# Kernel tuning notes

Measured on AMD Instinct MI355X. Metric: run time of the kernel, lower is better.

The kernel has to match this reference:

```python
import jax, jax.numpy as jnp
import numpy as np

N = 10000   # nodes
E = 320000  # edges
G = 64      # graphs in batch
D = 256     # gnn embedding dim
A = 118     # atomic_num_dim
OUT = 100   # spectrum dim
NUM_GINE = 2


def setup_inputs() -> dict:
    key = jax.random.key(0)
    ks = jax.random.split(key, 16)
    inp = {
        'atomic_num': jax.random.normal(ks[0], (N, A), dtype=jnp.float32),
        'length': jax.random.uniform(ks[1], (E,), dtype=jnp.float32),
        'src': jax.random.randint(ks[2], (E,), 0, N, dtype=jnp.int32),
        'dst': jax.random.randint(ks[3], (E,), 0, N, dtype=jnp.int32),
        'graph_ids': jnp.sort(jax.random.randint(ks[4], (N,), 0, G, dtype=jnp.int32)),
        # parameters
        'W_node': jax.random.normal(ks[5], (A, D), dtype=jnp.float32) / np.sqrt(A),
        'b_node': jnp.zeros((D,), dtype=jnp.float32),
        'W_edge': jax.random.normal(ks[6], (1, D), dtype=jnp.float32),
        'b_edge': jnp.zeros((D,), dtype=jnp.float32),
        'gine_eps': jnp.zeros((NUM_GINE,), dtype=jnp.float32),  # learnable eps per GINEConv
        'W_gnn': jax.random.normal(ks[7], (NUM_GINE, D, D), dtype=jnp.float32) / np.sqrt(D),
        'b_gnn': jnp.zeros((NUM_GINE, D), dtype=jnp.float32),
        'eps_param': jnp.array([1e-3], dtype=jnp.float32),  # unify_vector eps
        'W_mlp': jax.random.normal(ks[8], (D, OUT), dtype=jnp.float32) / np.sqrt(D),
        'b_mlp': jnp.zeros((OUT,), dtype=jnp.float32),
    }
    return inp


def reference(atomic_num, length, src, dst, graph_ids,
              W_node, b_node, W_edge, b_edge,
              gine_eps, W_gnn, b_gnn, eps_param, W_mlp, b_mlp):
    # node / edge embeddings
    h = atomic_num @ W_node + b_node            # [N, D]
    e = length[:, None] @ W_edge + b_edge       # [E, D]
    # GINEConv layers: m_ij = relu(h_src + e_ij); h_i' = W((1+eps)h_i + sum_j m_ij) + b
    for i in range(NUM_GINE):
        m = jax.nn.relu(h[src] + e)             # [E, D] gather + elementwise
        agg = jax.ops.segment_sum(m, dst, num_segments=N)  # scatter-sum to dst nodes
        h = ((1.0 + gine_eps[i]) * h + agg) @ W_gnn[i] + b_gnn[i]
    # sum_nodes pooling per graph
    feat = jax.ops.segment_sum(h, graph_ids, num_segments=G)  # [G, D]
    # unify_vector: global min/max normalization
    mn = jnp.min(feat)
    mx = jnp.max(feat)
    feat = (feat - mn) / (eps_param[0] + mx - mn)
    # MLP head (no hidden layers): Linear(D, 100)
    return feat @ W_mlp + b_mlp                 # [G, 100]
```

## Files before the change

kernel.cpp:

```cpp
#include <hip/hip_runtime.h>
#include <hip/hip_bf16.h>

#define N_NODES 10000
#define N_EDGES 320000
#define N_GRAPHS 64
#define DIM 256
#define HALF_D 128
#define ADIM 118
#define OUTD 100
#define CAP 192

typedef short bf8_t __attribute__((ext_vector_type(8)));
typedef float f4_t  __attribute__((ext_vector_type(4)));

__device__ __forceinline__ unsigned short f2bf(float f) {
    unsigned u = __float_as_uint(f);
    u += 0x7FFFu + ((u >> 16) & 1u);
    return (unsigned short)(u >> 16);
}
__device__ __forceinline__ float bf2f(unsigned short s) {
    return __uint_as_float(((unsigned)s) << 16);
}

__global__ __launch_bounds__(256) void convW_k(
    const float* __restrict__ Wn, const float* __restrict__ Wg,
    unsigned short* __restrict__ WnT, unsigned short* __restrict__ WgT,
    int* __restrict__ cursor, float* __restrict__ feat) {
    int i = blockIdx.x * 256 + threadIdx.x;
    if (i < 32768) {
        int c = i >> 7, k = i & 127;
        WnT[i] = (k < ADIM) ? f2bf(Wn[k * DIM + c]) : (unsigned short)0;
    } else {
        int j = i - 32768;
        int l = j >> 16, rem = j & 65535;
        int c = rem >> 8, k = rem & 255;
        WgT[j] = f2bf(Wg[l * 65536 + k * DIM + c]);
    }
    if (i < N_NODES) cursor[i] = i * CAP;
    if (i < N_GRAPHS * DIM) feat[i] = 0.f;
}

__global__ __launch_bounds__(256) void fill_k(
    const int* __restrict__ src, const int* __restrict__ dst,
    const float* __restrict__ len, int* __restrict__ cursor,
    int2* __restrict__ epack) {
    int j = blockIdx.x * 256 + threadIdx.x;
    if (j >= N_EDGES) return;
    int d = dst[j];
    int pos = atomicAdd(&cursor[d], 1);
    if (pos < d * CAP + CAP)
        epack[pos] = make_int2(src[j], __float_as_int(len[j]));
}

#define AST 136
__global__ __launch_bounds__(256) void node_embed_k(
    const float* __restrict__ an, const unsigned short* __restrict__ WnT,
    const float* __restrict__ bn, unsigned short* __restrict__ hbf) {
    __shared__ unsigned short xs[16 * AST];
    const int base = blockIdx.x * 16;
    const int tid = threadIdx.x;
    for (int i = tid; i < 16 * (AST - ADIM); i += 256) {
        int r = i / (AST - ADIM);
        int c = i - r * (AST - ADIM);
        xs[r * AST + ADIM + c] = 0;
    }
    for (int i = tid; i < 16 * ADIM; i += 256) {
        int r = i / ADIM;
        int c = i - r * ADIM;
        xs[r * AST + c] = f2bf(an[(size_t)(base + r) * ADIM + c]);
    }
    __syncthreads();
    const int wave = tid >> 6, lane = tid & 63;
    const int m = lane & 15, quad = lane >> 4;
    bf8_t afrag[4];
    #pragma unroll
    for (int s = 0; s < 4; ++s)
        afrag[s] = *(const bf8_t*)&xs[m * AST + s * 32 + quad * 8];
    const int colbase = wave * 64;
    f4_t acc[4];
    #pragma unroll
    for (int ct = 0; ct < 4; ++ct) acc[ct] = (f4_t){0.f, 0.f, 0.f, 0.f};
    #pragma unroll
    for (int ct = 0; ct < 4; ++ct) {
        const unsigned short* wp = WnT + (size_t)(colbase + ct * 16 + m) * 128 + quad * 8;
        #pragma unroll
        for (int s = 0; s < 4; ++s) {
            bf8_t bfrag = *(const bf8_t*)(wp + s * 32);
            acc[ct] = __builtin_amdgcn_mfma_f32_16x16x32_bf16(afrag[s], bfrag, acc[ct], 0, 0, 0);
        }
    }
    #pragma unroll
    for (int ct = 0; ct < 4; ++ct) {
        int col = colbase + ct * 16 + m;
        float bb = bn[col];
        unsigned short* hp = hbf + (size_t)(col >> 7) * N_NODES * HALF_D + (col & 127);
        #pragma unroll
        for (int r = 0; r < 4; ++r)
            hp[(size_t)(base + quad * 4 + r) * HALF_D] = f2bf(acc[ct][r] + bb);
    }
}

__global__ __launch_bounds__(256) void gather_k(
    const unsigned short* __restrict__ hbf, const int* __restrict__ cursor,
    const int2* __restrict__ epack, const float* __restrict__ We,
    const float* __restrict__ be, const float* __restrict__ epsp, int layer,
    unsigned short* __restrict__ xbf) {
    const int wave = threadIdx.x >> 6, lane = threadIdx.x & 63;
    const int q = blockIdx.x >> 3, r = blockIdx.x & 7;
    const int half = r >> 2;
    const int node = __builtin_amdgcn_readfirstlane((q * 4 + (r & 3)) * 4 + wave);
    const int d = half * HALF_D + lane * 2;
    const unsigned short* hb = hbf + (size_t)half * N_NODES * HALF_D + lane * 2;
    const float2 w  = *(const float2*)(We + d);
    const float2 bb = *(const float2*)(be + d);
    float2 acc = {0.f, 0.f};
    const int lo = node * CAP;
    const int cnt = min(__builtin_amdgcn_readfirstlane(cursor[node]) - lo, CAP);
    const int2* ep = epack + lo;
    int t = 0;
    for (; t + 7 < cnt; t += 8) {
        int2 p0 = ep[t + 0], p1 = ep[t + 1], p2 = ep[t + 2], p3 = ep[t + 3];
        int2 p4 = ep[t + 4], p5 = ep[t + 5], p6 = ep[t + 6], p7 = ep[t + 7];
        ushort2 a0 = *(const ushort2*)(hb + (size_t)p0.x * HALF_D);
        ushort2 a1 = *(const ushort2*)(hb + (size_t)p1.x * HALF_D);
        ushort2 a2 = *(const ushort2*)(hb + (size_t)p2.x * HALF_D);
        ushort2 a3 = *(const ushort2*)(hb + (size_t)p3.x * HALF_D);
        ushort2 a4 = *(const ushort2*)(hb + (size_t)p4.x * HALF_D);
        ushort2 a5 = *(const ushort2*)(hb + (size_t)p5.x * HALF_D);
        ushort2 a6 = *(const ushort2*)(hb + (size_t)p6.x * HALF_D);
        ushort2 a7 = *(const ushort2*)(hb + (size_t)p7.x * HALF_D);
        float l0 = __int_as_float(p0.y), l1 = __int_as_float(p1.y);
        float l2 = __int_as_float(p2.y), l3 = __int_as_float(p3.y);
        float l4 = __int_as_float(p4.y), l5 = __int_as_float(p5.y);
        float l6 = __int_as_float(p6.y), l7 = __int_as_float(p7.y);
        acc.x += fmaxf(bf2f(a0.x) + fmaf(l0, w.x, bb.x), 0.f);
        acc.y += fmaxf(bf2f(a0.y) + fmaf(l0, w.y, bb.y), 0.f);
        acc.x += fmaxf(bf2f(a1.x) + fmaf(l1, w.x, bb.x), 0.f);
        acc.y += fmaxf(bf2f(a1.y) + fmaf(l1, w.y, bb.y), 0.f);
        acc.x += fmaxf(bf2f(a2.x) + fmaf(l2, w.x, bb.x), 0.f);
        acc.y += fmaxf(bf2f(a2.y) + fmaf(l2, w.y, bb.y), 0.f);
        acc.x += fmaxf(bf2f(a3.x) + fmaf(l3, w.x, bb.x), 0.f);
        acc.y += fmaxf(bf2f(a3.y) + fmaf(l3, w.y, bb.y), 0.f);
        acc.x += fmaxf(bf2f(a4.x) + fmaf(l4, w.x, bb.x), 0.f);
        acc.y += fmaxf(bf2f(a4.y) + fmaf(l4, w.y, bb.y), 0.f);
        acc.x += fmaxf(bf2f(a5.x) + fmaf(l5, w.x, bb.x), 0.f);
        acc.y += fmaxf(bf2f(a5.y) + fmaf(l5, w.y, bb.y), 0.f);
        acc.x += fmaxf(bf2f(a6.x) + fmaf(l6, w.x, bb.x), 0.f);
        acc.y += fmaxf(bf2f(a6.y) + fmaf(l6, w.y, bb.y), 0.f);
        acc.x += fmaxf(bf2f(a7.x) + fmaf(l7, w.x, bb.x), 0.f);
        acc.y += fmaxf(bf2f(a7.y) + fmaf(l7, w.y, bb.y), 0.f);
    }
    for (; t < cnt; ++t) {
        int2 p0 = ep[t];
        ushort2 a0 = *(const ushort2*)(hb + (size_t)p0.x * HALF_D);
        float l0 = __int_as_float(p0.y);
        acc.x += fmaxf(bf2f(a0.x) + fmaf(l0, w.x, bb.x), 0.f);
        acc.y += fmaxf(bf2f(a0.y) + fmaf(l0, w.y, bb.y), 0.f);
    }
    const float eps1 = 1.f + epsp[layer];
    ushort2 hv = *(const ushort2*)(hb + (size_t)node * HALF_D);
    ushort2 o;
    o.x = f2bf(fmaf(eps1, bf2f(hv.x), acc.x));
    o.y = f2bf(fmaf(eps1, bf2f(hv.y), acc.y));
    *(ushort2*)(xbf + (size_t)half * N_NODES * HALF_D + (size_t)node * HALF_D + lane * 2) = o;
}

#define XST 264
__global__ __launch_bounds__(256) void update_k(
    const unsigned short* __restrict__ xbf,
    const unsigned short* __restrict__ WT, const float* __restrict__ b,
    unsigned short* __restrict__ hout,
    const int* __restrict__ gid, float* __restrict__ feat, int do_pool) {
    __shared__ unsigned short xs[16 * XST];
    __shared__ int gids[16];
    const int base = blockIdx.x * 16;
    const int tid = threadIdx.x;
    #pragma unroll
    for (int cch = tid; cch < 512; cch += 256) {
        int rr = cch >> 5, k0 = (cch & 31) * 8;
        const unsigned short* sp = xbf + (size_t)(k0 >> 7) * N_NODES * HALF_D
                                 + (size_t)(base + rr) * HALF_D + (k0 & 127);
        *(bf8_t*)&xs[rr * XST + k0] = *(const bf8_t*)sp;
    }
    if (do_pool && tid < 16) gids[tid] = gid[base + tid];
    __syncthreads();
    const int wave = tid >> 6, lane = tid & 63;
    const int m = lane & 15, quad = lane >> 4;
    bf8_t afrag[8];
    #pragma unroll
    for (int s = 0; s < 8; ++s)
        afrag[s] = *(const bf8_t*)&xs[m * XST + s * 32 + quad * 8];
    const int colbase = wave * 64;
    f4_t acc[4];
    #pragma unroll
    for (int ct = 0; ct < 4; ++ct) acc[ct] = (f4_t){0.f, 0.f, 0.f, 0.f};
    #pragma unroll
    for (int ct = 0; ct < 4; ++ct) {
        const unsigned short* wp = WT + (size_t)(colbase + ct * 16 + m) * DIM + quad * 8;
        #pragma unroll
        for (int s = 0; s < 8; ++s) {
            bf8_t bfrag = *(const bf8_t*)(wp + s * 32);
            acc[ct] = __builtin_amdgcn_mfma_f32_16x16x32_bf16(afrag[s], bfrag, acc[ct], 0, 0, 0);
        }
    }
    if (!do_pool) {
        #pragma unroll
        for (int ct = 0; ct < 4; ++ct) {
            int col = colbase + ct * 16 + m;
            float bb = b[col];
            unsigned short* hp = hout + (size_t)(col >> 7) * N_NODES * HALF_D + (col & 127);
            #pragma unroll
            for (int r = 0; r < 4; ++r)
                hp[(size_t)(base + quad * 4 + r) * HALF_D] = f2bf(acc[ct][r] + bb);
        }
    } else {
        #pragma unroll
        for (int ct = 0; ct < 4; ++ct) {
            int col = colbase + ct * 16 + m;
            float bb = b[col];
            float run = 0.f;
            int cur = gids[quad * 4];
            #pragma unroll
            for (int r = 0; r < 4; ++r) {
                int g = gids[quad * 4 + r];
                if (g != cur) {
                    atomicAdd(&feat[(size_t)cur * DIM + col], run);
                    run = 0.f;
                    cur = g;
                }
                run += acc[ct][r] + bb;
            }
            atomicAdd(&feat[(size_t)cur * DIM + col], run);
        }
    }
}

__global__ __launch_bounds__(256) void headmm_k(
    const float* __restrict__ feat, const float* __restrict__ Wm,
    const float* __restrict__ bm, const float* __restrict__ epsp,
    float* __restrict__ out) {
    __shared__ float frow[DIM];
    __shared__ float smn[4], smx[4], sMn, sMx;
    const int g = blockIdx.x;
    const int tid = threadIdx.x;
    float mn = 3.4e38f, mx = -3.4e38f;
    for (int i = tid; i < N_GRAPHS * DIM; i += 256) {
        float v = feat[i];
        mn = fminf(mn, v);
        mx = fmaxf(mx, v);
    }
    frow[tid] = feat[g * DIM + tid];
    #pragma unroll
    for (int off = 32; off > 0; off >>= 1) {
        mn = fminf(mn, __shfl_down(mn, off, 64));
        mx = fmaxf(mx, __shfl_down(mx, off, 64));
    }
    const int wave = tid >> 6, lane = tid & 63;
    if (lane == 0) { smn[wave] = mn; smx[wave] = mx; }
    __syncthreads();
    if (tid == 0) {
        sMn = fminf(fminf(smn[0], smn[1]), fminf(smn[2], smn[3]));
        sMx = fmaxf(fmaxf(smx[0], smx[1]), fmaxf(smx[2], smx[3]));
    }
    __syncthreads();
    if (tid < OUTD) {
        const float mnv = sMn;
        const float inv = 1.f / (epsp[0] + sMx - mnv);
        float acc = 0.f;
        for (int d = 0; d < DIM; ++d)
            acc += (frow[d] - mnv) * Wm[d * OUTD + tid];
        out[g * OUTD + tid] = acc * inv + bm[tid];
    }
}

extern "C" void kernel_launch(void* const* d_in, const int* in_sizes, int n_in,
                              void* d_out, int out_size, void* d_ws, size_t ws_size,
                              hipStream_t stream) {
    const float* atomic_num = (const float*)d_in[0];
    const float* length     = (const float*)d_in[1];
    const int*   src        = (const int*)d_in[2];
    const int*   dst        = (const int*)d_in[3];
    const int*   gid        = (const int*)d_in[4];
    const float* W_node     = (const float*)d_in[5];
    const float* b_node     = (const float*)d_in[6];
    const float* W_edge     = (const float*)d_in[7];
    const float* b_edge     = (const float*)d_in[8];
    const float* gine_eps   = (const float*)d_in[9];
    const float* W_gnn      = (const float*)d_in[10];
    const float* b_gnn      = (const float*)d_in[11];
    const float* eps_param  = (const float*)d_in[12];
    const float* W_mlp      = (const float*)d_in[13];
    const float* b_mlp      = (const float*)d_in[14];
    float* out = (float*)d_out;

    float* feat = (float*)d_ws;
    int* cursor = (int*)(feat + (size_t)N_GRAPHS * DIM);
    int2* epack = (int2*)(cursor + N_NODES + 4);
    unsigned short* hbf0 = (unsigned short*)(epack + (size_t)N_NODES * CAP);
    unsigned short* hbf1 = hbf0 + (size_t)N_NODES * DIM;
    unsigned short* xbf  = hbf1 + (size_t)N_NODES * DIM;
    unsigned short* WnT  = xbf + (size_t)N_NODES * DIM;
    unsigned short* WgT  = WnT + 256 * 128;

    convW_k<<<640, 256, 0, stream>>>(W_node, W_gnn, WnT, WgT, cursor, feat);
    fill_k<<<N_EDGES / 256, 256, 0, stream>>>(src, dst, length, cursor, epack);
    node_embed_k<<<N_NODES / 16, 256, 0, stream>>>(atomic_num, WnT, b_node, hbf0);

    gather_k<<<N_NODES / 2, 256, 0, stream>>>(
        hbf0, cursor, epack, W_edge, b_edge, gine_eps, 0, xbf);
    update_k<<<N_NODES / 16, 256, 0, stream>>>(
        xbf, WgT, b_gnn, hbf1, gid, feat, 0);
    gather_k<<<N_NODES / 2, 256, 0, stream>>>(
        hbf1, cursor, epack, W_edge, b_edge, gine_eps, 1, xbf);
    update_k<<<N_NODES / 16, 256, 0, stream>>>(
        xbf, WgT + 256 * 256, b_gnn + DIM, hbf0, gid, feat, 1);

    headmm_k<<<N_GRAPHS, 256, 0, stream>>>(feat, W_mlp, b_mlp, eps_param, out);
}
```

Measured before the change: 217.4 us.

## Switch node features to row-major layout and split edges across waves per node

Node feature buffers move from a split-half column layout to plain row-major [N, 256] bf16. The gather kernel now gives each node its own block: the four waves each take a quarter of the node's edges, each lane loads 4 contiguous bf16 values per edge, and the partial sums are reduced through shared memory. The update kernel splits each 16-row tile across two blocks, each computing 128 output columns, to raise parallelism. The aim is wider, full-row gathers and better load balance across waves, paid for with an extra shared-memory reduction, a barrier per node and twice as many gather blocks.

```diff
diff --git a/kernel.cpp b/kernel.cpp
--- a/kernel.cpp
+++ b/kernel.cpp
@@ -5,7 +5,6 @@
 #define N_EDGES 320000
 #define N_GRAPHS 64
 #define DIM 256
-#define HALF_D 128
 #define ADIM 118
 #define OUTD 100
 #define CAP 192
@@ -93,10 +92,9 @@
     for (int ct = 0; ct < 4; ++ct) {
         int col = colbase + ct * 16 + m;
         float bb = bn[col];
-        unsigned short* hp = hbf + (size_t)(col >> 7) * N_NODES * HALF_D + (col & 127);
         #pragma unroll
         for (int r = 0; r < 4; ++r)
-            hp[(size_t)(base + quad * 4 + r) * HALF_D] = f2bf(acc[ct][r] + bb);
+            hbf[(size_t)(base + quad * 4 + r) * DIM + col] = f2bf(acc[ct][r] + bb);
     }
 }
 
@@ -105,64 +103,61 @@
     const int2* __restrict__ epack, const float* __restrict__ We,
     const float* __restrict__ be, const float* __restrict__ epsp, int layer,
     unsigned short* __restrict__ xbf) {
+    __shared__ float sacc[4][DIM];
+    const int node = blockIdx.x;
     const int wave = threadIdx.x >> 6, lane = threadIdx.x & 63;
-    const int q = blockIdx.x >> 3, r = blockIdx.x & 7;
-    const int half = r >> 2;
-    const int node = __builtin_amdgcn_readfirstlane((q * 4 + (r & 3)) * 4 + wave);
-    const int d = half * HALF_D + lane * 2;
-    const unsigned short* hb = hbf + (size_t)half * N_NODES * HALF_D + lane * 2;
-    const float2 w  = *(const float2*)(We + d);
-    const float2 bb = *(const float2*)(be + d);
-    float2 acc = {0.f, 0.f};
+    const int c = lane << 2;
+    const float4 w  = *(const float4*)(We + c);
+    const float4 bb = *(const float4*)(be + c);
     const int lo = node * CAP;
-    const int cnt = min(__builtin_amdgcn_readfirstlane(cursor[node]) - lo, CAP);
+    const int cnt = min(cursor[node] - lo, CAP);
+    const int chunk = (cnt + 3) >> 2;
+    const int t0 = wave * chunk;
+    const int t1 = min(cnt, t0 + chunk);
+    float4 acc = {0.f, 0.f, 0.f, 0.f};
     const int2* ep = epack + lo;
-    int t = 0;
-    for (; t + 7 < cnt; t += 8) {
-        int2 p0 = ep[t + 0], p1 = ep[t + 1], p2 = ep[t + 2], p3 = ep[t + 3];
-        int2 p4 = ep[t + 4], p5 = ep[t + 5], p6 = ep[t + 6], p7 = ep[t + 7];
-        ushort2 a0 = *(const ushort2*)(hb + (size_t)p0.x * HALF_D);
-        ushort2 a1 = *(const ushort2*)(hb + (size_t)p1.x * HALF_D);
-        ushort2 a2 = *(const ushort2*)(hb + (size_t)p2.x * HALF_D);
-        ushort2 a3 = *(const ushort2*)(hb + (size_t)p3.x * HALF_D);
-        ushort2 a4 = *(const ushort2*)(hb + (size_t)p4.x * HALF_D);
-        ushort2 a5 = *(const ushort2*)(hb + (size_t)p5.x * HALF_D);
-        ushort2 a6 = *(const ushort2*)(hb + (size_t)p6.x * HALF_D);
-        ushort2 a7 = *(const ushort2*)(hb + (size_t)p7.x * HALF_D);
+    int t = t0;
+    for (; t + 3 < t1; t += 4) {
+        int2 p0 = ep[t], p1 = ep[t + 1], p2 = ep[t + 2], p3 = ep[t + 3];
+        ushort4 a0 = *(const ushort4*)(hbf + (size_t)p0.x * DIM + c);
+        ushort4 a1 = *(const ushort4*)(hbf + (size_t)p1.x * DIM + c);
+        ushort4 a2 = *(const ushort4*)(hbf + (size_t)p2.x * DIM + c);
+        ushort4 a3 = *(const ushort4*)(hbf + (size_t)p3.x * DIM + c);
         float l0 = __int_as_float(p0.y), l1 = __int_as_float(p1.y);
         float l2 = __int_as_float(p2.y), l3 = __int_as_float(p3.y);
-        float l4 = __int_as_float(p4.y), l5 = __int_as_float(p5.y);
-        float l6 = __int_as_float(p6.y), l7 = __int_as_float(p7.y);
         acc.x += fmaxf(bf2f(a0.x) + fmaf(l0, w.x, bb.x), 0.f);
         acc.y += fmaxf(bf2f(a0.y) + fmaf(l0, w.y, bb.y), 0.f);
+        acc.z += fmaxf(bf2f(a0.z) + fmaf(l0, w.z, bb.z), 0.f);
+        acc.w += fmaxf(bf2f(a0.w) + fmaf(l0, w.w, bb.w), 0.f);
         acc.x += fmaxf(bf2f(a1.x) + fmaf(l1, w.x, bb.x), 0.f);
         acc.y += fmaxf(bf2f(a1.y) + fmaf(l1, w.y, bb.y), 0.f);
+        acc.z += fmaxf(bf2f(a1.z) + fmaf(l1, w.z, bb.z), 0.f);
+        acc.w += fmaxf(bf2f(a1.w) + fmaf(l1, w.w, bb.w), 0.f);
         acc.x += fmaxf(bf2f(a2.x) + fmaf(l2, w.x, bb.x), 0.f);
         acc.y += fmaxf(bf2f(a2.y) + fmaf(l2, w.y, bb.y), 0.f);
+        acc.z += fmaxf(bf2f(a2.z) + fmaf(l2, w.z, bb.z), 0.f);
+        acc.w += fmaxf(bf2f(a2.w) + fmaf(l2, w.w, bb.w), 0.f);
         acc.x += fmaxf(bf2f(a3.x) + fmaf(l3, w.x, bb.x), 0.f);
         acc.y += fmaxf(bf2f(a3.y) + fmaf(l3, w.y, bb.y), 0.f);
-        acc.x += fmaxf(bf2f(a4.x) + fmaf(l4, w.x, bb.x), 0.f);
-        acc.y += fmaxf(bf2f(a4.y) + fmaf(l4, w.y, bb.y), 0.f);
-        acc.x += fmaxf(bf2f(a5.x) + fmaf(l5, w.x, bb.x), 0.f);
-        acc.y += fmaxf(bf2f(a5.y) + fmaf(l5, w.y, bb.y), 0.f);
-        acc.x += fmaxf(bf2f(a6.x) + fmaf(l6, w.x, bb.x), 0.f);
-        acc.y += fmaxf(bf2f(a6.y) + fmaf(l6, w.y, bb.y), 0.f);
-        acc.x += fmaxf(bf2f(a7.x) + fmaf(l7, w.x, bb.x), 0.f);
-        acc.y += fmaxf(bf2f(a7.y) + fmaf(l7, w.y, bb.y), 0.f);
-    }
-    for (; t < cnt; ++t) {
+        acc.z += fmaxf(bf2f(a3.z) + fmaf(l3, w.z, bb.z), 0.f);
+        acc.w += fmaxf(bf2f(a3.w) + fmaf(l3, w.w, bb.w), 0.f);
+    }
+    for (; t < t1; ++t) {
         int2 p0 = ep[t];
-        ushort2 a0 = *(const ushort2*)(hb + (size_t)p0.x * HALF_D);
+        ushort4 a0 = *(const ushort4*)(hbf + (size_t)p0.x * DIM + c);
         float l0 = __int_as_float(p0.y);
         acc.x += fmaxf(bf2f(a0.x) + fmaf(l0, w.x, bb.x), 0.f);
         acc.y += fmaxf(bf2f(a0.y) + fmaf(l0, w.y, bb.y), 0.f);
-    }
+        acc.z += fmaxf(bf2f(a0.z) + fmaf(l0, w.z, bb.z), 0.f);
+        acc.w += fmaxf(bf2f(a0.w) + fmaf(l0, w.w, bb.w), 0.f);
+    }
+    *(float4*)&sacc[wave][c] = acc;
+    __syncthreads();
+    const int d = threadIdx.x;
+    float s = sacc[0][d] + sacc[1][d] + sacc[2][d] + sacc[3][d];
     const float eps1 = 1.f + epsp[layer];
-    ushort2 hv = *(const ushort2*)(hb + (size_t)node * HALF_D);
-    ushort2 o;
-    o.x = f2bf(fmaf(eps1, bf2f(hv.x), acc.x));
-    o.y = f2bf(fmaf(eps1, bf2f(hv.y), acc.y));
-    *(ushort2*)(xbf + (size_t)half * N_NODES * HALF_D + (size_t)node * HALF_D + lane * 2) = o;
+    float hv = bf2f(hbf[(size_t)node * DIM + d]);
+    xbf[(size_t)node * DIM + d] = f2bf(fmaf(eps1, hv, s));
 }
 
 #define XST 264
@@ -173,14 +168,14 @@
     const int* __restrict__ gid, float* __restrict__ feat, int do_pool) {
     __shared__ unsigned short xs[16 * XST];
     __shared__ int gids[16];
-    const int base = blockIdx.x * 16;
+    const int rb = blockIdx.x >> 1;
+    const int halfc = blockIdx.x & 1;
+    const int base = rb * 16;
     const int tid = threadIdx.x;
     #pragma unroll
     for (int cch = tid; cch < 512; cch += 256) {
         int rr = cch >> 5, k0 = (cch & 31) * 8;
-        const unsigned short* sp = xbf + (size_t)(k0 >> 7) * N_NODES * HALF_D
-                                 + (size_t)(base + rr) * HALF_D + (k0 & 127);
-        *(bf8_t*)&xs[rr * XST + k0] = *(const bf8_t*)sp;
+        *(bf8_t*)&xs[rr * XST + k0] = *(const bf8_t*)(xbf + (size_t)(base + rr) * DIM + k0);
     }
     if (do_pool && tid < 16) gids[tid] = gid[base + tid];
     __syncthreads();
@@ -190,12 +185,12 @@
     #pragma unroll
     for (int s = 0; s < 8; ++s)
         afrag[s] = *(const bf8_t*)&xs[m * XST + s * 32 + quad * 8];
-    const int colbase = wave * 64;
-    f4_t acc[4];
-    #pragma unroll
-    for (int ct = 0; ct < 4; ++ct) acc[ct] = (f4_t){0.f, 0.f, 0.f, 0.f};
-    #pragma unroll
-    for (int ct = 0; ct < 4; ++ct) {
+    const int colbase = halfc * 128 + wave * 32;
+    f4_t acc[2];
+    #pragma unroll
+    for (int ct = 0; ct < 2; ++ct) acc[ct] = (f4_t){0.f, 0.f, 0.f, 0.f};
+    #pragma unroll
+    for (int ct = 0; ct < 2; ++ct) {
         const unsigned short* wp = WT + (size_t)(colbase + ct * 16 + m) * DIM + quad * 8;
         #pragma unroll
         for (int s = 0; s < 8; ++s) {
@@ -205,17 +200,16 @@
     }
     if (!do_pool) {
         #pragma unroll
-        for (int ct = 0; ct < 4; ++ct) {
+        for (int ct = 0; ct < 2; ++ct) {
             int col = colbase + ct * 16 + m;
             float bb = b[col];
-            unsigned short* hp = hout + (size_t)(col >> 7) * N_NODES * HALF_D + (col & 127);
             #pragma unroll
             for (int r = 0; r < 4; ++r)
-                hp[(size_t)(base + quad * 4 + r) * HALF_D] = f2bf(acc[ct][r] + bb);
+                hout[(size_t)(base + quad * 4 + r) * DIM + col] = f2bf(acc[ct][r] + bb);
         }
     } else {
         #pragma unroll
-        for (int ct = 0; ct < 4; ++ct) {
+        for (int ct = 0; ct < 2; ++ct) {
             int col = colbase + ct * 16 + m;
             float bb = b[col];
             float run = 0.f;
@@ -306,13 +300,13 @@
     fill_k<<<N_EDGES / 256, 256, 0, stream>>>(src, dst, length, cursor, epack);
     node_embed_k<<<N_NODES / 16, 256, 0, stream>>>(atomic_num, WnT, b_node, hbf0);
 
-    gather_k<<<N_NODES / 2, 256, 0, stream>>>(
+    gather_k<<<N_NODES, 256, 0, stream>>>(
         hbf0, cursor, epack, W_edge, b_edge, gine_eps, 0, xbf);
-    update_k<<<N_NODES / 16, 256, 0, stream>>>(
+    update_k<<<(N_NODES / 16) * 2, 256, 0, stream>>>(
         xbf, WgT, b_gnn, hbf1, gid, feat, 0);
-    gather_k<<<N_NODES / 2, 256, 0, stream>>>(
+    gather_k<<<N_NODES, 256, 0, stream>>>(
         hbf1, cursor, epack, W_edge, b_edge, gine_eps, 1, xbf);
-    update_k<<<N_NODES / 16, 256, 0, stream>>>(
+    update_k<<<(N_NODES / 16) * 2, 256, 0, stream>>>(
         xbf, WgT + 256 * 256, b_gnn + DIM, hbf0, gid, feat, 1);
 
     headmm_k<<<N_GRAPHS, 256, 0, stream>>>(feat, W_mlp, b_mlp, eps_param, out);
```

Result: slower. 230.7 us (+6.1%).
